# Kernel tuning notes

Hardware: AMD Instinct MI355X
Metric: run time of the kernel (lower is better)

Reference implementation:

```python
import jax, jax.numpy as jnp
import numpy as np

BETA = 0.25
COMMIT_W = 1.0
EPS = 1e-6
N_E, E_DIM, C = 8192, 256, 256
B, H, W = 16, 32, 32


def setup_inputs() -> dict:
    key = jax.random.key(0)
    k1, k2, k3 = jax.random.split(key, 3)
    z = jax.random.normal(k1, (B, C, H, W), jnp.float32)
    frozen_codebook = jax.random.normal(k2, (N_E, E_DIM), jnp.float32) * (E_DIM ** -0.5)
    w_transform = jax.random.normal(k3, (C, E_DIM), jnp.float32) * (E_DIM ** -0.5)
    return {"z": z, "frozen_codebook": frozen_codebook, "w_transform": w_transform}


def _rotate_to(src, tgt):
    # Rotation trick: Householder-style rotation of src onto direction of tgt.
    sg = jax.lax.stop_gradient
    norm_src = jnp.linalg.norm(src, axis=-1, keepdims=True)
    norm_tgt = jnp.linalg.norm(tgt, axis=-1, keepdims=True)
    u = src / jnp.clip(norm_src, EPS)          # normalized source
    q = tgt / jnp.clip(norm_tgt, EPS)          # normalized target
    w = u + q
    w = sg(w / jnp.clip(jnp.linalg.norm(w, axis=-1, keepdims=True), EPS))
    u = sg(u)
    q = sg(q)
    e = src  # gradients flow through e only (rotation matrix is detached)
    rotated = (e
               - 2.0 * jnp.sum(e * w, axis=-1, keepdims=True) * w
               + 2.0 * jnp.sum(e * u, axis=-1, keepdims=True) * q)
    return rotated * sg(norm_tgt / jnp.clip(norm_src, EPS))


def reference(z, frozen_codebook, w_transform):
    z = z.astype(jnp.float32)
    zc = jnp.transpose(z, (0, 2, 3, 1))          # b h w c
    z_flat = zc.reshape(-1, zc.shape[-1])        # [N, C]
    codebook = frozen_codebook @ w_transform.T   # [n_e, C] (Linear, no bias)

    # squared L2 distances, argmin under no_grad
    d = (jnp.sum(z_flat ** 2, axis=1, keepdims=True)
         + jnp.sum(codebook ** 2, axis=1)
         - 2.0 * jnp.einsum('bd,nd->bn', z_flat, codebook))
    indices = jnp.argmin(jax.lax.stop_gradient(d), axis=1)  # [N]

    z_q_flat = codebook[indices]                 # [N, C]
    sg = jax.lax.stop_gradient
    loss = (jnp.mean((sg(z_flat) - z_q_flat) ** 2)
            + BETA * jnp.mean((z_flat - sg(z_q_flat)) ** 2)) * COMMIT_W

    z_q_flat = _rotate_to(z_flat, z_q_flat)      # rotation trick
    z_q = z_q_flat.reshape(zc.shape)             # b h w c
    z_q = jnp.transpose(z_q, (0, 3, 1, 2))       # b c h w
    return z_q, loss, indices
```

## Files before the change

### kernel.cpp

```cpp
#include <hip/hip_runtime.h>
#include <math.h>

typedef unsigned short u16;
typedef unsigned int   u32;

#define B_   16
#define C_   256
#define HW_  1024
#define N_   16384
#define NE_  8192
#define K_   256
#define NSPLIT 8
#define CPS  1024
#define NZQ  4194304

typedef _Float16 f16x8 __attribute__((ext_vector_type(8)));
typedef float    f32x16 __attribute__((ext_vector_type(16)));


__device__ __forceinline__ u16 f2h(float x) {
    union { _Float16 h; u16 u; } c;
    c.h = (_Float16)x;
    return c.u;
}

__global__ void k_transpose_z(const float* __restrict__ z, float* __restrict__ zf,
                              u16* __restrict__ zh) {
    __shared__ float tile[32][33];
    int b   = blockIdx.z;
    int hw0 = blockIdx.x * 32;
    int c0  = blockIdx.y * 32;
    int tx = threadIdx.x;
    int ty = threadIdx.y;
    #pragma unroll
    for (int i = 0; i < 4; ++i) {
        int c = c0 + ty + i * 8;
        tile[ty + i * 8][tx] = z[((size_t)b * C_ + c) * HW_ + hw0 + tx];
    }
    __syncthreads();
    #pragma unroll
    for (int i = 0; i < 4; ++i) {
        int hw = hw0 + ty + i * 8;
        size_t o = ((size_t)b * HW_ + hw) * C_ + c0 + tx;
        float v = tile[tx][ty + i * 8];
        zf[o] = v;
        zh[o] = f2h(v);
    }
}

__global__ __launch_bounds__(256) void k_codebook_gemm(
        const float* __restrict__ f, const float* __restrict__ w,
        float* __restrict__ cb, u16* __restrict__ cbh) {
    __shared__ float Fs[16][68];
    __shared__ float Ws[16][68];
    int n0 = blockIdx.x * 64;
    int c0 = blockIdx.y * 64;
    int tid = threadIdx.x;
    int tx = tid & 15, ty = tid >> 4;
    int nl = tid >> 2;
    int kq = (tid & 3) * 4;
    float acc[4][4] = {};
    for (int kb = 0; kb < K_; kb += 16) {
        float4 fv = *(const float4*)&f[(size_t)(n0 + nl) * K_ + kb + kq];
        float4 wv = *(const float4*)&w[(size_t)(c0 + nl) * K_ + kb + kq];
        __syncthreads();
        Fs[kq + 0][nl] = fv.x; Fs[kq + 1][nl] = fv.y; Fs[kq + 2][nl] = fv.z; Fs[kq + 3][nl] = fv.w;
        Ws[kq + 0][nl] = wv.x; Ws[kq + 1][nl] = wv.y; Ws[kq + 2][nl] = wv.z; Ws[kq + 3][nl] = wv.w;
        __syncthreads();
        #pragma unroll
        for (int k = 0; k < 16; ++k) {
            float4 a = *(float4*)&Fs[k][ty * 4];
            float4 b = *(float4*)&Ws[k][tx * 4];
            float av[4] = {a.x, a.y, a.z, a.w};
            float bv[4] = {b.x, b.y, b.z, b.w};
            #pragma unroll
            for (int i = 0; i < 4; ++i)
                #pragma unroll
                for (int j = 0; j < 4; ++j)
                    acc[i][j] += av[i] * bv[j];
        }
    }
    #pragma unroll
    for (int i = 0; i < 4; ++i) {
        size_t o = (size_t)(n0 + ty * 4 + i) * K_ + c0 + tx * 4;
        *(float4*)&cb[o] = make_float4(acc[i][0], acc[i][1], acc[i][2], acc[i][3]);
        *(ushort4*)&cbh[o] = make_ushort4(f2h(acc[i][0]), f2h(acc[i][1]),
                                          f2h(acc[i][2]), f2h(acc[i][3]));
    }
}

__global__ void k_c2(const float* __restrict__ cb, float* __restrict__ c2,
                     double* __restrict__ c2d) {
    int row  = blockIdx.x * 4 + (threadIdx.x >> 6);
    int lane = threadIdx.x & 63;
    float4 v = *(const float4*)&cb[(size_t)row * K_ + lane * 4];
    double s = (double)v.x * v.x + (double)v.y * v.y
             + (double)v.z * v.z + (double)v.w * v.w;
    #pragma unroll
    for (int off = 32; off; off >>= 1) s += __shfl_down(s, off, 64);
    if (lane == 0) { c2d[row] = s; c2[row] = (float)(s * 8192.0 + 262144.0); }
}

__device__ __forceinline__ void ld_lds16(const void* g, void* l) {
    __builtin_amdgcn_global_load_lds((const __attribute__((address_space(1))) void*)g,
                                     (__attribute__((address_space(3))) void*)l, 16, 0, 0);
}

#define INS(M1, M2, U) { u32 t_ = min(M1, U); u32 h_ = max(M1, U); M1 = t_; M2 = min(M2, h_); }

#define SCORE16(ACC, M1, M2, CGBASE, C2B) do {                                  \
    u32 ib_ = (u32)(code0 + (CGBASE));                                          \
    _Pragma("unroll")                                                           \
    for (int h = 0; h < 4; ++h) {                                               \
        float4 cv = *(const float4*)&(C2B)[(CGBASE) + 8 * h];                   \
        u32 s0 = (u32)fmaxf(fmaf(-16384.f, (ACC)[4*h+0], cv.x), 0.f);           \
        u32 s1 = (u32)fmaxf(fmaf(-16384.f, (ACC)[4*h+1], cv.y), 0.f);           \
        u32 s2 = (u32)fmaxf(fmaf(-16384.f, (ACC)[4*h+2], cv.z), 0.f);           \
        u32 s3 = (u32)fmaxf(fmaf(-16384.f, (ACC)[4*h+3], cv.w), 0.f);           \
        u32 u0 = (s0 << 13) + ib_ + 8*h + 0;                                    \
        u32 u1 = (s1 << 13) + ib_ + 8*h + 1;                                    \
        u32 u2 = (s2 << 13) + ib_ + 8*h + 2;                                    \
        u32 u3 = (s3 << 13) + ib_ + 8*h + 3;                                    \
        INS(M1, M2, u0); INS(M1, M2, u1); INS(M1, M2, u2); INS(M1, M2, u3);     \
    }                                                                           \
} while (0)

__global__ __launch_bounds__(256, 2) void k_scan_mfma(
        const u16* __restrict__ zh, const u16* __restrict__ cbh,
        const float* __restrict__ c2, int* __restrict__ t2i) {
    __shared__ __align__(16) u16 sA[2][8192];
    __shared__ __align__(16) u16 sB[2][8192];
    __shared__ __align__(16) float c2s[2][128];

    int r0    = blockIdx.x * 128;
    int split = blockIdx.y;
    int tid  = threadIdx.x;
    int wave = tid >> 6, lane = tid & 63;
    int l31 = lane & 31, q = lane >> 5;

    int ra = ((wave & 1) << 6) + l31;
    int rb = ((wave >> 1) << 6) + l31;

    u32 m1a = 0xFFFFFFFFu, m2a = 0xFFFFFFFFu;
    u32 m1b = 0xFFFFFFFFu, m2b = 0xFFFFFFFFu;

    auto STAGE = [&](int s) {
        int ct = s >> 2, kbo = (s & 3) * 64;
        int c0 = split * CPS + ct * 128;
        const u16* Ab = cbh + (size_t)c0 * K_ + kbo;
        const u16* Bb = zh  + (size_t)r0 * K_ + kbo;
        u16* sAb = &sA[s & 1][0];
        u16* sBb = &sB[s & 1][0];
        #pragma unroll
        for (int it = 0; it < 4; ++it) {
            int S = (it * 4 + wave) * 64 + lane;
            int row = S >> 3, u = S & 7;
            int k8 = (u ^ (row & 7)) * 8;
            size_t goff = (size_t)row * K_ + k8;
            u32 loff = (u32)(it * 4 + wave) * 512;
            ld_lds16(Ab + goff, sAb + loff);
            ld_lds16(Bb + goff, sBb + loff);
        }
        if ((s & 3) == 0 && tid < 32)
            ld_lds16(&c2[c0 + tid * 4], &c2s[ct & 1][tid * 4]);
    };

    f32x16 acc0 = (f32x16){}, acc1 = (f32x16){}, acc2 = (f32x16){}, acc3 = (f32x16){};
    STAGE(0);
    __syncthreads();

    for (int s = 0; s < 32; ++s) {
        int ct = s >> 2, kb = s & 3;
        if (s + 1 < 32) STAGE(s + 1);
        const u16* sAb = &sA[s & 1][0];
        const u16* sBb = &sB[s & 1][0];
        #pragma unroll
        for (int ks = 0; ks < 4; ++ks) {
            u32 u8 = (u32)(((ks * 2 + q) ^ (l31 & 7)) * 8);
            f16x8 af0 = *(const f16x8*)&sAb[(u32)ra * 64 + u8];
            f16x8 af1 = *(const f16x8*)&sAb[(u32)ra * 64 + 2048 + u8];
            f16x8 bf0 = *(const f16x8*)&sBb[(u32)rb * 64 + u8];
            f16x8 bf1 = *(const f16x8*)&sBb[(u32)rb * 64 + 2048 + u8];
            acc0 = __builtin_amdgcn_mfma_f32_32x32x16_f16(af0, bf0, acc0, 0, 0, 0);
            acc1 = __builtin_amdgcn_mfma_f32_32x32x16_f16(af1, bf0, acc1, 0, 0, 0);
            acc2 = __builtin_amdgcn_mfma_f32_32x32x16_f16(af0, bf1, acc2, 0, 0, 0);
            acc3 = __builtin_amdgcn_mfma_f32_32x32x16_f16(af1, bf1, acc3, 0, 0, 0);
        }
        if (kb == 3) {
            int code0 = split * CPS + ct * 128;
            const float* C2B = &c2s[ct & 1][0];
            int cga = ((wave & 1) << 6) + (q << 2);
            int cgb = cga + 32;
            SCORE16(acc0, m1a, m2a, cga, C2B);
            SCORE16(acc1, m1a, m2a, cgb, C2B);
            SCORE16(acc2, m1b, m2b, cga, C2B);
            SCORE16(acc3, m1b, m2b, cgb, C2B);
            acc0 = (f32x16){}; acc1 = (f32x16){}; acc2 = (f32x16){}; acc3 = (f32x16){};
        }
        __syncthreads();
    }

    {
        u32 o1 = __shfl_xor(m1a, 32, 64), o2 = __shfl_xor(m2a, 32, 64);
        u32 h = max(m1a, o1); m1a = min(m1a, o1); m2a = min(min(m2a, o2), h);
        o1 = __shfl_xor(m1b, 32, 64); o2 = __shfl_xor(m2b, 32, 64);
        h = max(m1b, o1); m1b = min(m1b, o1); m2b = min(min(m2b, o2), h);
    }
    u32* mbuf = (u32*)&sA[0][0];
    if (q == 0) {
        int base = ((wave * 2 + 0) * 32 + l31) * 2;
        mbuf[base] = m1a; mbuf[base + 1] = m2a;
        base = ((wave * 2 + 1) * 32 + l31) * 2;
        mbuf[base] = m1b; mbuf[base + 1] = m2b;
    }
    __syncthreads();
    if (tid < 128) {
        int zr = tid, wp = zr >> 6, zg = (zr >> 5) & 1, l = zr & 31;
        int iA = (((wp * 2 + 0) * 2 + zg) * 32 + l) * 2;
        int iB = (((wp * 2 + 1) * 2 + zg) * 32 + l) * 2;
        u32 a1 = mbuf[iA], a2 = mbuf[iA + 1];
        u32 b1 = mbuf[iB], b2 = mbuf[iB + 1];
        u32 h  = max(a1, b1), f1 = min(a1, b1);
        u32 f2 = min(min(a2, b2), h);
        size_t o = ((size_t)split * N_ + (r0 + zr)) * 2;
        t2i[o] = (int)(f1 & 0x1FFFu);
        t2i[o + 1] = (int)(f2 & 0x1FFFu);
    }
}

__global__ __launch_bounds__(256) void k_finalize(
        const float* __restrict__ zf, const float* __restrict__ cb,
        const double* __restrict__ c2d, const int* __restrict__ t2i,
        float* __restrict__ out, float* __restrict__ partials) {
    __shared__ int   bidx[16];
    __shared__ float wsum[4];
    __shared__ float tile[16][260];
    int n0 = blockIdx.x * 16;
    int tid = threadIdx.x;
    int wv = tid >> 6, lane = tid & 63;
    int h = lane >> 5, l5 = lane & 31;

    for (int rr = 0; rr < 4; ++rr) {
        int n = n0 + wv * 4 + rr;
        double bs = 1e300; int bi = 0x7fffffff;
        for (int p = 0; p < 8; ++p) {
            int t = 2 * p + h;
            int sp = t >> 1, wsel = t & 1;
            int ci = t2i[((size_t)sp * N_ + n) * 2 + wsel];
            double acc = 0.0;
            const float* zp = zf + (size_t)n * K_;
            const float* cp = cb + (size_t)ci * K_;
            #pragma unroll
            for (int jj = 0; jj < 2; ++jj) {
                float4 zv = *(const float4*)&zp[l5 * 4 + jj * 128];
                float4 cv = *(const float4*)&cp[l5 * 4 + jj * 128];
                acc += (double)zv.x * cv.x + (double)zv.y * cv.y
                     + (double)zv.z * cv.z + (double)zv.w * cv.w;
            }
            #pragma unroll
            for (int off = 1; off < 32; off <<= 1) acc += __shfl_xor(acc, off, 32);
            double sc = c2d[ci] - 2.0 * acc;
            double so = __shfl_xor(sc, 32, 64);
            int    io = __shfl_xor(ci, 32, 64);
            double s0 = h ? so : sc;  int i0 = h ? io : ci;
            double s1 = h ? sc : so;  int i1 = h ? ci : io;
            if (s0 < bs || (s0 == bs && i0 < bi)) { bs = s0; bi = i0; }
            if (s1 < bs || (s1 == bs && i1 < bi)) { bs = s1; bi = i1; }
        }
        if (lane == 0) {
            bidx[wv * 4 + rr] = bi;
            out[(size_t)NZQ + 1 + n] = (float)bi;
        }
    }
    __syncthreads();

    float accl = 0.f;
    for (int l = 0; l < 16; ++l) {
        int n = n0 + l;
        int bi = bidx[l];
        float zq = cb[(size_t)bi * K_ + tid];
        float d  = zf[(size_t)n * K_ + tid] - zq;
        accl += d * d;
        tile[l][tid] = zq;
    }
    #pragma unroll
    for (int off = 32; off; off >>= 1) accl += __shfl_down(accl, off, 64);
    if ((tid & 63) == 0) wsum[tid >> 6] = accl;
    __syncthreads();
    if (tid == 0) partials[blockIdx.x] = wsum[0] + wsum[1] + wsum[2] + wsum[3];
    int b = n0 >> 10, hw0 = n0 & 1023;
    #pragma unroll
    for (int g = 0; g < 4; ++g) {
        float4 v = make_float4(tile[g * 4 + 0][tid], tile[g * 4 + 1][tid],
                               tile[g * 4 + 2][tid], tile[g * 4 + 3][tid]);
        *(float4*)&out[((size_t)b * C_ + tid) * HW_ + hw0 + g * 4] = v;
    }
}

__global__ void k_loss(const float* __restrict__ partials, float* __restrict__ out) {
    __shared__ double ws4[4];
    int tid = threadIdx.x;
    double s = 0.0;
    for (int i = tid; i < 1024; i += 256) s += (double)partials[i];
    #pragma unroll
    for (int off = 32; off; off >>= 1) s += __shfl_down(s, off, 64);
    if ((tid & 63) == 0) ws4[tid >> 6] = s;
    __syncthreads();
    if (tid == 0) {
        double tot = ws4[0] + ws4[1] + ws4[2] + ws4[3];
        out[NZQ] = (float)(1.25 * tot / (double)NZQ);
    }
}

extern "C" void kernel_launch(void* const* d_in, const int* in_sizes, int n_in,
                              void* d_out, int out_size, void* d_ws, size_t ws_size,
                              hipStream_t stream) {
    const float* z  = (const float*)d_in[0];
    const float* fc = (const float*)d_in[1];
    const float* wt = (const float*)d_in[2];
    float* out = (float*)d_out;

    float* ws = (float*)d_ws;
    const size_t OFF_ZF   = 0;
    const size_t OFF_CB   = OFF_ZF + (size_t)N_ * K_;
    const size_t OFF_C2   = OFF_CB + (size_t)NE_ * K_;
    const size_t OFF_C2D  = OFF_C2 + NE_;
    const size_t OFF_T2I  = OFF_C2D + (size_t)NE_ * 2;
    const size_t OFF_PART = OFF_T2I + (size_t)NSPLIT * N_ * 2;
    const size_t OFF_ZH   = OFF_PART + 1024;
    const size_t OFF_CBH  = OFF_ZH + (size_t)N_ * K_ / 2;

    float*  zf   = ws + OFF_ZF;
    float*  cb   = ws + OFF_CB;
    float*  c2   = ws + OFF_C2;
    double* c2d  = (double*)(ws + OFF_C2D);
    int*    t2i  = (int*)(ws + OFF_T2I);
    float*  part = ws + OFF_PART;
    u16*    zh   = (u16*)(ws + OFF_ZH);
    u16*    cbh  = (u16*)(ws + OFF_CBH);

    k_transpose_z<<<dim3(HW_ / 32, C_ / 32, B_), dim3(32, 8), 0, stream>>>(z, zf, zh);
    k_codebook_gemm<<<dim3(NE_ / 64, K_ / 64), 256, 0, stream>>>(fc, wt, cb, cbh);
    k_c2<<<NE_ / 4, 256, 0, stream>>>(cb, c2, c2d);
    k_scan_mfma<<<dim3(N_ / 128, NSPLIT), 256, 0, stream>>>(zh, cbh, c2, t2i);
    k_finalize<<<N_ / 16, 256, 0, stream>>>(zf, cb, c2d, t2i, out, part);
    k_loss<<<1, 256, 0, stream>>>(part, out);
}
```

Before: 241.6 us.

## Keep z tile in registers, stream only codebook through LDS in scan kernel

The scan kernel now loads each wave's z fragments (full K=256) into registers once, instead of restaging them through LDS on every step. Only codebook tiles are double-buffered via global_load_lds, which halves LDS traffic and LDS footprint. It also adds s_setprio around the MFMA block and rescales the quantized score (half scale, no clamp) to save an instruction per element. The cost is about 64 more VGPRs per thread, which puts pressure on the 2-block launch bound and risks spills. The coarser score scale could also change near-tie argmin results.

Result: faster. 226.3 us (-6.3%).

```diff
diff --git a/kernel.cpp b/kernel.cpp
--- a/kernel.cpp
+++ b/kernel.cpp
@@ -98,7 +98,7 @@
              + (double)v.z * v.z + (double)v.w * v.w;
     #pragma unroll
     for (int off = 32; off; off >>= 1) s += __shfl_down(s, off, 64);
-    if (lane == 0) { c2d[row] = s; c2[row] = (float)(s * 8192.0 + 262144.0); }
+    if (lane == 0) { c2d[row] = s; c2[row] = (float)(s * 4096.0 + 262144.0); }
 }
 
 __device__ __forceinline__ void ld_lds16(const void* g, void* l) {
@@ -108,28 +108,23 @@
 
 #define INS(M1, M2, U) { u32 t_ = min(M1, U); u32 h_ = max(M1, U); M1 = t_; M2 = min(M2, h_); }
 
-#define SCORE16(ACC, M1, M2, CGBASE, C2B) do {                                  \
-    u32 ib_ = (u32)(code0 + (CGBASE));                                          \
-    _Pragma("unroll")                                                           \
-    for (int h = 0; h < 4; ++h) {                                               \
-        float4 cv = *(const float4*)&(C2B)[(CGBASE) + 8 * h];                   \
-        u32 s0 = (u32)fmaxf(fmaf(-16384.f, (ACC)[4*h+0], cv.x), 0.f);           \
-        u32 s1 = (u32)fmaxf(fmaf(-16384.f, (ACC)[4*h+1], cv.y), 0.f);           \
-        u32 s2 = (u32)fmaxf(fmaf(-16384.f, (ACC)[4*h+2], cv.z), 0.f);           \
-        u32 s3 = (u32)fmaxf(fmaf(-16384.f, (ACC)[4*h+3], cv.w), 0.f);           \
-        u32 u0 = (s0 << 13) + ib_ + 8*h + 0;                                    \
-        u32 u1 = (s1 << 13) + ib_ + 8*h + 1;                                    \
-        u32 u2 = (s2 << 13) + ib_ + 8*h + 2;                                    \
-        u32 u3 = (s3 << 13) + ib_ + 8*h + 3;                                    \
-        INS(M1, M2, u0); INS(M1, M2, u1); INS(M1, M2, u2); INS(M1, M2, u3);     \
-    }                                                                           \
+#define SCORE16(ACC, M1, M2, CGBASE, C2B) do {                                    \
+    u32 ib_ = (u32)(code0 + (CGBASE));                                            \
+    _Pragma("unroll")                                                             \
+    for (int h = 0; h < 4; ++h) {                                                 \
+        float4 cv = *(const float4*)&(C2B)[(CGBASE) + 8 * h];                     \
+        u32 u0 = (((u32)fmaf(-8192.f, (ACC)[4*h+0], cv.x)) << 13) + ib_ + 8*h + 0; \
+        u32 u1 = (((u32)fmaf(-8192.f, (ACC)[4*h+1], cv.y)) << 13) + ib_ + 8*h + 1; \
+        u32 u2 = (((u32)fmaf(-8192.f, (ACC)[4*h+2], cv.z)) << 13) + ib_ + 8*h + 2; \
+        u32 u3 = (((u32)fmaf(-8192.f, (ACC)[4*h+3], cv.w)) << 13) + ib_ + 8*h + 3; \
+        INS(M1, M2, u0); INS(M1, M2, u1); INS(M1, M2, u2); INS(M1, M2, u3);       \
+    }                                                                             \
 } while (0)
 
 __global__ __launch_bounds__(256, 2) void k_scan_mfma(
         const u16* __restrict__ zh, const u16* __restrict__ cbh,
         const float* __restrict__ c2, int* __restrict__ t2i) {
     __shared__ __align__(16) u16 sA[2][8192];
-    __shared__ __align__(16) u16 sB[2][8192];
     __shared__ __align__(16) float c2s[2][128];
 
     int r0    = blockIdx.x * 128;
@@ -137,67 +132,80 @@
     int tid  = threadIdx.x;
     int wave = tid >> 6, lane = tid & 63;
     int l31 = lane & 31, q = lane >> 5;
-
     int ra = ((wave & 1) << 6) + l31;
-    int rb = ((wave >> 1) << 6) + l31;
+
+    const u16* zp = zh + (size_t)(r0 + ((wave >> 1) << 6) + l31) * K_ + q * 8;
+    f16x8 zr0[16], zr1[16];
+    #pragma unroll
+    for (int t = 0; t < 16; ++t) {
+        zr0[t] = *(const f16x8*)&zp[t * 16];
+        zr1[t] = *(const f16x8*)&zp[32 * K_ + t * 16];
+    }
+
+    size_t ga[4]; u32 la[4];
+    #pragma unroll
+    for (int it = 0; it < 4; ++it) {
+        int S = (it * 4 + wave) * 64 + lane;
+        int row = S >> 3, u = S & 7;
+        ga[it] = (size_t)row * K_ + (u ^ (row & 7)) * 8;
+        la[it] = (u32)(it * 4 + wave) * 512;
+    }
 
     u32 m1a = 0xFFFFFFFFu, m2a = 0xFFFFFFFFu;
     u32 m1b = 0xFFFFFFFFu, m2b = 0xFFFFFFFFu;
 
-    auto STAGE = [&](int s) {
-        int ct = s >> 2, kbo = (s & 3) * 64;
-        int c0 = split * CPS + ct * 128;
-        const u16* Ab = cbh + (size_t)c0 * K_ + kbo;
-        const u16* Bb = zh  + (size_t)r0 * K_ + kbo;
-        u16* sAb = &sA[s & 1][0];
-        u16* sBb = &sB[s & 1][0];
+    const u16* cb0 = cbh + (size_t)split * CPS * K_;
+
+    {
         #pragma unroll
-        for (int it = 0; it < 4; ++it) {
-            int S = (it * 4 + wave) * 64 + lane;
-            int row = S >> 3, u = S & 7;
-            int k8 = (u ^ (row & 7)) * 8;
-            size_t goff = (size_t)row * K_ + k8;
-            u32 loff = (u32)(it * 4 + wave) * 512;
-            ld_lds16(Ab + goff, sAb + loff);
-            ld_lds16(Bb + goff, sBb + loff);
+        for (int it = 0; it < 4; ++it) ld_lds16(cb0 + ga[it], &sA[0][la[it]]);
+        if (tid < 32) ld_lds16(&c2[split * CPS + tid * 4], &c2s[0][0]);
+    }
+    __syncthreads();
+
+    f32x16 acc0 = (f32x16){}, acc1 = (f32x16){}, acc2 = (f32x16){}, acc3 = (f32x16){};
+    for (int ct = 0; ct < 8; ++ct) {
+        int code0 = split * CPS + ct * 128;
+        const u16* Act = cb0 + (size_t)(ct * 128) * K_;
+        #pragma unroll
+        for (int kb = 0; kb < 4; ++kb) {
+            if (kb < 3) {
+                const u16* Ab = Act + (kb + 1) * 64;
+                u16* d = &sA[(kb + 1) & 1][0];
+                #pragma unroll
+                for (int it = 0; it < 4; ++it) ld_lds16(Ab + ga[it], d + la[it]);
+            } else if (ct < 7) {
+                const u16* Ab = Act + (size_t)128 * K_;
+                u16* d = &sA[0][0];
+                #pragma unroll
+                for (int it = 0; it < 4; ++it) ld_lds16(Ab + ga[it], d + la[it]);
+                if (tid < 32) ld_lds16(&c2[code0 + 128 + tid * 4], &c2s[(ct + 1) & 1][0]);
+            }
+            const u16* sAb = &sA[kb & 1][0];
+            __builtin_amdgcn_s_setprio(1);
+            #pragma unroll
+            for (int ks = 0; ks < 4; ++ks) {
+                u32 u8 = (u32)(((ks * 2 + q) ^ (l31 & 7)) * 8);
+                f16x8 af0 = *(const f16x8*)&sAb[(u32)ra * 64 + u8];
+                f16x8 af1 = *(const f16x8*)&sAb[(u32)ra * 64 + 2048 + u8];
+                acc0 = __builtin_amdgcn_mfma_f32_32x32x16_f16(af0, zr0[kb * 4 + ks], acc0, 0, 0, 0);
+                acc1 = __builtin_amdgcn_mfma_f32_32x32x16_f16(af1, zr0[kb * 4 + ks], acc1, 0, 0, 0);
+                acc2 = __builtin_amdgcn_mfma_f32_32x32x16_f16(af0, zr1[kb * 4 + ks], acc2, 0, 0, 0);
+                acc3 = __builtin_amdgcn_mfma_f32_32x32x16_f16(af1, zr1[kb * 4 + ks], acc3, 0, 0, 0);
+            }
+            __builtin_amdgcn_s_setprio(0);
+            if (kb == 3) {
+                const float* C2B = &c2s[ct & 1][0];
+                int cga = ((wave & 1) << 6) + (q << 2);
+                int cgb = cga + 32;
+                SCORE16(acc0, m1a, m2a, cga, C2B);
+                SCORE16(acc1, m1a, m2a, cgb, C2B);
+                SCORE16(acc2, m1b, m2b, cga, C2B);
+                SCORE16(acc3, m1b, m2b, cgb, C2B);
+                acc0 = (f32x16){}; acc1 = (f32x16){}; acc2 = (f32x16){}; acc3 = (f32x16){};
+            }
+            __syncthreads();
         }
-        if ((s & 3) == 0 && tid < 32)
-            ld_lds16(&c2[c0 + tid * 4], &c2s[ct & 1][tid * 4]);
-    };
-
-    f32x16 acc0 = (f32x16){}, acc1 = (f32x16){}, acc2 = (f32x16){}, acc3 = (f32x16){};
-    STAGE(0);
-    __syncthreads();
-
-    for (int s = 0; s < 32; ++s) {
-        int ct = s >> 2, kb = s & 3;
-        if (s + 1 < 32) STAGE(s + 1);
-        const u16* sAb = &sA[s & 1][0];
-        const u16* sBb = &sB[s & 1][0];
-        #pragma unroll
-        for (int ks = 0; ks < 4; ++ks) {
-            u32 u8 = (u32)(((ks * 2 + q) ^ (l31 & 7)) * 8);
-            f16x8 af0 = *(const f16x8*)&sAb[(u32)ra * 64 + u8];
-            f16x8 af1 = *(const f16x8*)&sAb[(u32)ra * 64 + 2048 + u8];
-            f16x8 bf0 = *(const f16x8*)&sBb[(u32)rb * 64 + u8];
-            f16x8 bf1 = *(const f16x8*)&sBb[(u32)rb * 64 + 2048 + u8];
-            acc0 = __builtin_amdgcn_mfma_f32_32x32x16_f16(af0, bf0, acc0, 0, 0, 0);
-            acc1 = __builtin_amdgcn_mfma_f32_32x32x16_f16(af1, bf0, acc1, 0, 0, 0);
-            acc2 = __builtin_amdgcn_mfma_f32_32x32x16_f16(af0, bf1, acc2, 0, 0, 0);
-            acc3 = __builtin_amdgcn_mfma_f32_32x32x16_f16(af1, bf1, acc3, 0, 0, 0);
-        }
-        if (kb == 3) {
-            int code0 = split * CPS + ct * 128;
-            const float* C2B = &c2s[ct & 1][0];
-            int cga = ((wave & 1) << 6) + (q << 2);
-            int cgb = cga + 32;
-            SCORE16(acc0, m1a, m2a, cga, C2B);
-            SCORE16(acc1, m1a, m2a, cgb, C2B);
-            SCORE16(acc2, m1b, m2b, cga, C2B);
-            SCORE16(acc3, m1b, m2b, cgb, C2B);
-            acc0 = (f32x16){}; acc1 = (f32x16){}; acc2 = (f32x16){}; acc3 = (f32x16){};
-        }
-        __syncthreads();
     }
 
     {
```
